# Optimization experiments

Measured on AMD Instinct MI355X. Metric: run time of the kernel, lower is better.

The kernel has to match this reference:

```python
import jax, jax.numpy as jnp
import numpy as np

B, SQ, SK = 2, 2048, 2048
D_MODEL, N_HEADS = 1024, 16
D_HEAD = D_MODEL // N_HEADS
LN_EPS = 1e-5


def _ln(x, w, b):
    # per-head LayerNorm over last dim (d_head)
    mu = jnp.mean(x, axis=-1, keepdims=True)
    var = jnp.mean(jnp.square(x - mu), axis=-1, keepdims=True)
    return (x - mu) * jax.lax.rsqrt(var + LN_EPS) * w + b


def setup_inputs() -> dict:
    key = jax.random.key(0)
    ks = jax.random.split(key, 8)
    sd = 1.0 / np.sqrt(D_MODEL)
    so = 1.0 / np.sqrt(D_HEAD)
    return {
        "x_q": jax.random.normal(ks[0], (B, SQ, D_MODEL), jnp.float32),
        "x_kv": jax.random.normal(ks[1], (B, SK, D_MODEL), jnp.float32),
        "mask": jnp.tril(jnp.ones((SQ, SK), dtype=bool)),  # causal
        "W_Q": jax.random.normal(ks[2], (N_HEADS, D_MODEL, D_HEAD), jnp.float32) * sd,
        "W_K": jax.random.normal(ks[3], (N_HEADS, D_MODEL, D_HEAD), jnp.float32) * sd,
        "W_V": jax.random.normal(ks[4], (N_HEADS, D_MODEL, D_HEAD), jnp.float32) * sd,
        "W_O": jax.random.normal(ks[5], (N_HEADS, D_HEAD, D_MODEL), jnp.float32) * so,
        "b_Q": jnp.zeros((N_HEADS, D_HEAD), jnp.float32),
        "b_K": jnp.zeros((N_HEADS, D_HEAD), jnp.float32),
        "b_V": jnp.zeros((N_HEADS, D_HEAD), jnp.float32),
        "b_O": jnp.zeros((D_MODEL,), jnp.float32),
        "ln1_w": jnp.ones((D_HEAD,), jnp.float32),
        "ln1_b": jnp.zeros((D_HEAD,), jnp.float32),
        "ln2_w": jnp.ones((D_HEAD,), jnp.float32),
        "ln2_b": jnp.zeros((D_HEAD,), jnp.float32),
    }


def reference(x_q, x_kv, mask, W_Q, W_K, W_V, W_O, b_Q, b_K, b_V, b_O,
              ln1_w, ln1_b, ln2_w, ln2_b):
    # QKV projections: b s d, n d h -> b s n h
    q = jnp.einsum('bsd,ndh->bsnh', x_q, W_Q) + b_Q
    k = jnp.einsum('bsd,ndh->bsnh', x_kv, W_K) + b_K
    v = jnp.einsum('bsd,ndh->bsnh', x_kv, W_V) + b_V
    # QK-norm (ln_first=False, rope=None -> just apply LN after projections)
    q = _ln(q, ln1_w, ln1_b)
    k = _ln(k, ln2_w, ln2_b)
    # NOTE: no 1/sqrt(d_head) scaling, matching the original module
    att = jnp.einsum('bqnh,bknh->bnqk', q, k)
    att = jnp.where(mask, att, -jnp.inf)
    probas = jax.nn.softmax(att, axis=-1)
    z = jnp.einsum('bnqk,bknh->bqnh', probas, v)
    out = jnp.einsum('bqnh,nhd->bqd', z, W_O) + b_O
    return (out, k, v)
```

## Files before the change

kernel.cpp:

```cpp
#include <hip/hip_runtime.h>
#include <hip/hip_bf16.h>

#define B_   2
#define SQ_  2048
#define DM_  1024
#define NH_  16
#define DH_  64

typedef __attribute__((ext_vector_type(8))) short          bf16x8;
typedef __attribute__((ext_vector_type(8))) unsigned short u16x8;
typedef __attribute__((ext_vector_type(4))) float          f32x4;

__device__ __forceinline__ unsigned short f2bf(float f) {
    union { __hip_bfloat16 h; unsigned short u; } c;
    c.h = __float2bfloat16(f);
    return c.u;
}
__device__ __forceinline__ float gsum16(float v) {
    v += __shfl_xor(v, 1);
    v += __shfl_xor(v, 2);
    v += __shfl_xor(v, 4);
    v += __shfl_xor(v, 8);
    return v;
}

__global__ __launch_bounds__(256) void transpose_w(
    const float* __restrict__ src, unsigned short* __restrict__ dst, int R, int C)
{
    __shared__ float t[64][65];
    const int r0 = blockIdx.x * 64, c0 = blockIdx.y * 64;
    const size_t ms = (size_t)R * C * blockIdx.z;
    src += ms; dst += ms;
    const int lr = threadIdx.x >> 6, lc = threadIdx.x & 63;
#pragma unroll
    for (int i = 0; i < 16; ++i) {
        const int row = lr + i * 4;
        t[row][lc] = src[(size_t)(r0 + row) * C + c0 + lc];
    }
    __syncthreads();
#pragma unroll
    for (int i = 0; i < 16; ++i) {
        const int crow = lr + i * 4;
        dst[(size_t)(c0 + crow) * R + r0 + lc] = f2bf(t[lc][crow]);
    }
}

template <int TN, int A_BF16, int MODE>
__global__ __launch_bounds__(256) void mfma_gemm(
    const void* __restrict__ Asrc, const unsigned short* __restrict__ WT,
    const float* __restrict__ biasK, const float* __restrict__ biasV,
    const float* __restrict__ lnw, const float* __restrict__ lnb,
    float* __restrict__ Cf, float* __restrict__ Cf2,
    unsigned short* __restrict__ Cb, unsigned short* __restrict__ CbT)
{
    constexpr int MI = (TN == 128) ? 4 : 2;
    constexpr int BP = TN / 64;

    __shared__ __align__(16) unsigned short As[128][72];
    __shared__ __align__(16) unsigned short Bs[TN][72];

    const int tid = threadIdx.x;
    const int m0 = blockIdx.y * 128;
    const int c0 = blockIdx.x * TN;

    const int srow = tid >> 2;
    const int skc  = (tid & 3) * 16;

    float4 fa[2][4];
    u16x8  ba[2][2];
    u16x8  bb[BP][2];

    const int wid = tid >> 6, lane = tid & 63;
    const int wm = (TN == 128) ? (wid >> 1) * 64 : wid * 32;
    const int wn = (TN == 128) ? (wid & 1) * 64 : 0;
    const int l15 = lane & 15, qd = lane >> 4;

    const f32x4 zero4 = {0.f, 0.f, 0.f, 0.f};
    f32x4 acc[MI][4];
#pragma unroll
    for (int mi = 0; mi < MI; ++mi)
#pragma unroll
        for (int ni = 0; ni < 4; ++ni) acc[mi][ni] = zero4;

#define LOAD_A(kb)                                                              \
    {                                                                           \
        const size_t kof = (size_t)(kb) * 64 + skc;                             \
        if constexpr (!A_BF16) {                                                \
            const float* A = (const float*)Asrc;                                \
            for (int p = 0; p < 2; ++p) {                                       \
                const float* s = A + (size_t)(m0 + srow + p * 64) * 1024 + kof; \
                fa[p][0] = *(const float4*)(s + 0);                             \
                fa[p][1] = *(const float4*)(s + 4);                             \
                fa[p][2] = *(const float4*)(s + 8);                             \
                fa[p][3] = *(const float4*)(s + 12);                            \
            }                                                                   \
        } else {                                                                \
            const unsigned short* A = (const unsigned short*)Asrc;              \
            for (int p = 0; p < 2; ++p) {                                       \
                const unsigned short* s =                                       \
                    A + (size_t)(m0 + srow + p * 64) * 1024 + kof;              \
                ba[p][0] = *(const u16x8*)(s + 0);                              \
                ba[p][1] = *(const u16x8*)(s + 8);                              \
            }                                                                   \
        }                                                                       \
        for (int p = 0; p < BP; ++p) {                                          \
            const unsigned short* s =                                           \
                WT + (size_t)(c0 + srow + p * 64) * 1024 + kof;                 \
            bb[p][0] = *(const u16x8*)(s + 0);                                  \
            bb[p][1] = *(const u16x8*)(s + 8);                                  \
        }                                                                       \
    }

    LOAD_A(0)
    for (int kb = 0; kb < 16; ++kb) {
        __syncthreads();
#pragma unroll
        for (int p = 0; p < 2; ++p) {
            if constexpr (!A_BF16) {
                u16x8 lo, hi;
                lo[0] = f2bf(fa[p][0].x); lo[1] = f2bf(fa[p][0].y);
                lo[2] = f2bf(fa[p][0].z); lo[3] = f2bf(fa[p][0].w);
                lo[4] = f2bf(fa[p][1].x); lo[5] = f2bf(fa[p][1].y);
                lo[6] = f2bf(fa[p][1].z); lo[7] = f2bf(fa[p][1].w);
                hi[0] = f2bf(fa[p][2].x); hi[1] = f2bf(fa[p][2].y);
                hi[2] = f2bf(fa[p][2].z); hi[3] = f2bf(fa[p][2].w);
                hi[4] = f2bf(fa[p][3].x); hi[5] = f2bf(fa[p][3].y);
                hi[6] = f2bf(fa[p][3].z); hi[7] = f2bf(fa[p][3].w);
                *(u16x8*)&As[srow + p * 64][skc + 0] = lo;
                *(u16x8*)&As[srow + p * 64][skc + 8] = hi;
            } else {
                *(u16x8*)&As[srow + p * 64][skc + 0] = ba[p][0];
                *(u16x8*)&As[srow + p * 64][skc + 8] = ba[p][1];
            }
        }
#pragma unroll
        for (int p = 0; p < BP; ++p) {
            *(u16x8*)&Bs[srow + p * 64][skc + 0] = bb[p][0];
            *(u16x8*)&Bs[srow + p * 64][skc + 8] = bb[p][1];
        }
        __syncthreads();
        if (kb < 15) LOAD_A(kb + 1)
#pragma unroll
        for (int ks = 0; ks < 2; ++ks) {
            bf16x8 af[MI], bfr[4];
#pragma unroll
            for (int mi = 0; mi < MI; ++mi)
                af[mi] = *(const bf16x8*)&As[wm + mi * 16 + l15][ks * 32 + qd * 8];
#pragma unroll
            for (int ni = 0; ni < 4; ++ni)
                bfr[ni] = *(const bf16x8*)&Bs[wn + ni * 16 + l15][ks * 32 + qd * 8];
#pragma unroll
            for (int mi = 0; mi < MI; ++mi)
#pragma unroll
                for (int ni = 0; ni < 4; ++ni)
                    acc[mi][ni] = __builtin_amdgcn_mfma_f32_16x16x32_bf16(
                        af[mi], bfr[ni], acc[mi][ni], 0, 0, 0);
        }
    }
#undef LOAD_A

    const float* bias = (MODE == 1 && c0 >= 1024) ? biasV : biasK;
    float bv[4];
#pragma unroll
    for (int ni = 0; ni < 4; ++ni) bv[ni] = bias[(c0 + wn + ni * 16 + l15) & 1023];
#pragma unroll
    for (int mi = 0; mi < MI; ++mi)
#pragma unroll
        for (int ni = 0; ni < 4; ++ni)
#pragma unroll
            for (int r = 0; r < 4; ++r) acc[mi][ni][r] += bv[ni];

    if constexpr (MODE != 2) {
        const bool doLN = (MODE == 0) || (c0 < 1024);
        if (doLN) {
            float w4[4], lb4[4];
#pragma unroll
            for (int ni = 0; ni < 4; ++ni) {
                w4[ni]  = lnw[ni * 16 + l15];
                lb4[ni] = lnb[ni * 16 + l15];
            }
#pragma unroll
            for (int mi = 0; mi < MI; ++mi)
#pragma unroll
                for (int r = 0; r < 4; ++r) {
                    float s1 = acc[mi][0][r] + acc[mi][1][r] + acc[mi][2][r] + acc[mi][3][r];
                    const float mu = gsum16(s1) * (1.0f / 64.0f);
                    float s2 = acc[mi][0][r] * acc[mi][0][r] + acc[mi][1][r] * acc[mi][1][r]
                             + acc[mi][2][r] * acc[mi][2][r] + acc[mi][3][r] * acc[mi][3][r];
                    const float var = gsum16(s2) * (1.0f / 64.0f) - mu * mu;
                    const float rstd = rsqrtf(var + 1e-5f);
#pragma unroll
                    for (int ni = 0; ni < 4; ++ni)
                        acc[mi][ni][r] = (acc[mi][ni][r] - mu) * rstd * w4[ni] + lb4[ni];
                }
        }
    }

    if constexpr (MODE == 0) {
#pragma unroll
        for (int mi = 0; mi < MI; ++mi)
#pragma unroll
            for (int r = 0; r < 4; ++r) {
                const size_t grow = m0 + wm + mi * 16 + qd * 4 + r;
#pragma unroll
                for (int ni = 0; ni < 4; ++ni)
                    Cb[grow * 1024 + c0 + wn + ni * 16 + l15] = f2bf(acc[mi][ni][r]);
            }
    } else if constexpr (MODE == 2) {
#pragma unroll
        for (int mi = 0; mi < MI; ++mi)
#pragma unroll
            for (int r = 0; r < 4; ++r) {
                const size_t grow = m0 + wm + mi * 16 + qd * 4 + r;
#pragma unroll
                for (int ni = 0; ni < 4; ++ni)
                    Cf[grow * 1024 + c0 + wn + ni * 16 + l15] = acc[mi][ni][r];
            }
    } else {
        if (c0 < 1024) {
#pragma unroll
            for (int mi = 0; mi < MI; ++mi)
#pragma unroll
                for (int r = 0; r < 4; ++r) {
                    const size_t grow = m0 + wm + mi * 16 + qd * 4 + r;
#pragma unroll
                    for (int ni = 0; ni < 4; ++ni) {
                        const int gcol = c0 + wn + ni * 16 + l15;
                        Cf[grow * 1024 + gcol] = acc[mi][ni][r];
                        Cb[grow * 1024 + gcol] = f2bf(acc[mi][ni][r]);
                    }
                }
        } else {
#pragma unroll
            for (int mi = 0; mi < MI; ++mi) {
                const int growb = m0 + wm + mi * 16 + qd * 4;
                const int bb_ = growb >> 11, ss = growb & 2047;
#pragma unroll
                for (int ni = 0; ni < 4; ++ni) {
                    const int gv = c0 - 1024 + wn + ni * 16 + l15;
                    const int hh = gv >> 6, dd = gv & 63;
#pragma unroll
                    for (int r = 0; r < 4; ++r)
                        Cf2[(size_t)(growb + r) * 1024 + gv] = acc[mi][ni][r];
                    ushort4 w;
                    w.x = f2bf(acc[mi][ni][0]); w.y = f2bf(acc[mi][ni][1]);
                    w.z = f2bf(acc[mi][ni][2]); w.w = f2bf(acc[mi][ni][3]);
                    *(ushort4*)&CbT[(((size_t)bb_ * NH_ + hh) * DH_ + dd) * SQ_ + ss] = w;
                }
            }
        }
    }
}

__global__ __launch_bounds__(256) void attn_mfma(
    unsigned short* __restrict__ qz, const unsigned short* __restrict__ kbf,
    const unsigned short* __restrict__ vbfT)
{
    __shared__ __align__(16) unsigned short Ks[64][72];
    __shared__ __align__(16) unsigned short VsT[64][72];
    __shared__ __align__(16) unsigned short Ps[64][72];

    const int tid = threadIdx.x;
    const int h = blockIdx.y, b = blockIdx.z;
    const int wid = tid >> 6, lane = tid & 63;
    const int l15 = lane & 15, qd = lane >> 4;
    const int srow = tid >> 2, scol = (tid & 3) * 16;

    const size_t kbase = (size_t)b * SQ_ * DM_ + (size_t)h * DH_;
    const size_t vbase = ((size_t)b * NH_ + h) * DH_ * (size_t)SQ_;

    const f32x4 zero4 = {0.f, 0.f, 0.f, 0.f};

    for (int pass = 0; pass < 2; ++pass) {
        const int qt = pass ? blockIdx.x : (SQ_ / 64 - 1) - blockIdx.x;

        bf16x8 qf[2];
        {
            const unsigned short* qp =
                qz + kbase + (size_t)(qt * 64 + wid * 16 + l15) * DM_ + qd * 8;
            qf[0] = *(const bf16x8*)(qp);
            qf[1] = *(const bf16x8*)(qp + 32);
        }

        f32x4 z[4];
#pragma unroll
        for (int ni = 0; ni < 4; ++ni) z[ni] = zero4;
        float m_i = -3.0e38f, l_i = 0.f;

        for (int kt = 0; kt <= qt; ++kt) {
            __syncthreads();
            {
                const unsigned short* ks = kbf + kbase + (size_t)(kt * 64 + srow) * DM_ + scol;
                *(u16x8*)&Ks[srow][scol + 0] = *(const u16x8*)(ks + 0);
                *(u16x8*)&Ks[srow][scol + 8] = *(const u16x8*)(ks + 8);
                const unsigned short* vs = vbfT + vbase + (size_t)srow * SQ_ + kt * 64 + scol;
                *(u16x8*)&VsT[srow][scol + 0] = *(const u16x8*)(vs + 0);
                *(u16x8*)&VsT[srow][scol + 8] = *(const u16x8*)(vs + 8);
            }
            __syncthreads();

            f32x4 s[4];
#pragma unroll
            for (int mi = 0; mi < 4; ++mi) s[mi] = zero4;
#pragma unroll
            for (int ks = 0; ks < 2; ++ks) {
#pragma unroll
                for (int mi = 0; mi < 4; ++mi) {
                    const bf16x8 af = *(const bf16x8*)&Ks[mi * 16 + l15][ks * 32 + qd * 8];
                    s[mi] = __builtin_amdgcn_mfma_f32_16x16x32_bf16(af, qf[ks], s[mi], 0, 0, 0);
                }
            }

            if (kt == qt) {
#pragma unroll
                for (int mi = 0; mi < 4; ++mi)
#pragma unroll
                    for (int r = 0; r < 4; ++r)
                        if (mi * 16 + qd * 4 + r > wid * 16 + l15) s[mi][r] = -3.0e38f;
            }

            float mloc = -3.0e38f;
#pragma unroll
            for (int mi = 0; mi < 4; ++mi)
#pragma unroll
                for (int r = 0; r < 4; ++r) mloc = fmaxf(mloc, s[mi][r]);
            mloc = fmaxf(mloc, __shfl_xor(mloc, 16));
            mloc = fmaxf(mloc, __shfl_xor(mloc, 32));
            const float mn = fmaxf(m_i, mloc);
            const float alpha = __expf(m_i - mn);
            float rs = 0.f;
#pragma unroll
            for (int mi = 0; mi < 4; ++mi)
#pragma unroll
                for (int r = 0; r < 4; ++r) {
                    const float e = __expf(s[mi][r] - mn);
                    s[mi][r] = e;
                    rs += e;
                }
            rs += __shfl_xor(rs, 16);
            rs += __shfl_xor(rs, 32);
            l_i = l_i * alpha + rs;
            m_i = mn;

#pragma unroll
            for (int mi = 0; mi < 4; ++mi) {
                ushort4 w;
                w.x = f2bf(s[mi][0]); w.y = f2bf(s[mi][1]);
                w.z = f2bf(s[mi][2]); w.w = f2bf(s[mi][3]);
                *(ushort4*)&Ps[wid * 16 + l15][mi * 16 + qd * 4] = w;
            }

#pragma unroll
            for (int r = 0; r < 4; ++r) {
                const float ar = __shfl(alpha, qd * 4 + r);
#pragma unroll
                for (int ni = 0; ni < 4; ++ni) z[ni][r] *= ar;
            }

#pragma unroll
            for (int ks = 0; ks < 2; ++ks) {
                const bf16x8 ap = *(const bf16x8*)&Ps[wid * 16 + l15][ks * 32 + qd * 8];
#pragma unroll
                for (int ni = 0; ni < 4; ++ni) {
                    const bf16x8 bv = *(const bf16x8*)&VsT[ni * 16 + l15][ks * 32 + qd * 8];
                    z[ni] = __builtin_amdgcn_mfma_f32_16x16x32_bf16(ap, bv, z[ni], 0, 0, 0);
                }
            }
        }

        const float linv = 1.0f / l_i;
#pragma unroll
        for (int r = 0; r < 4; ++r) {
            const float lr_ = __shfl(linv, qd * 4 + r);
            const size_t row = (size_t)qt * 64 + wid * 16 + qd * 4 + r;
#pragma unroll
            for (int ni = 0; ni < 4; ++ni)
                qz[kbase + row * DM_ + ni * 16 + l15] = f2bf(z[ni][r] * lr_);
        }
    }
}

extern "C" void kernel_launch(void* const* d_in, const int* in_sizes, int n_in,
                              void* d_out, int out_size, void* d_ws, size_t ws_size,
                              hipStream_t stream)
{
    const float* x_q  = (const float*)d_in[0];
    const float* x_kv = (const float*)d_in[1];
    const float* W_Q  = (const float*)d_in[3];
    const float* W_K  = (const float*)d_in[4];
    const float* W_V  = (const float*)d_in[5];
    const float* W_O  = (const float*)d_in[6];
    const float* b_Q  = (const float*)d_in[7];
    const float* b_K  = (const float*)d_in[8];
    const float* b_V  = (const float*)d_in[9];
    const float* b_O  = (const float*)d_in[10];
    const float* ln1w = (const float*)d_in[11];
    const float* ln1b = (const float*)d_in[12];
    const float* ln2w = (const float*)d_in[13];
    const float* ln2b = (const float*)d_in[14];

    const size_t NTOK = (size_t)B_ * SQ_;
    float* out  = (float*)d_out;
    float* kout = out + NTOK * DM_;
    float* vout = kout + NTOK * DM_;

    unsigned short* wsu  = (unsigned short*)d_ws;
    unsigned short* WTq  = wsu;
    unsigned short* WTkv = WTq + (1u << 20);
    unsigned short* WTo  = WTkv + (2u << 20);
    unsigned short* qz   = WTo + (1u << 20);
    unsigned short* kbf  = qz + (1u << 22);
    unsigned short* vbfT = kbf + (1u << 22);

    transpose_w<<<dim3(16, 1, 16), 256, 0, stream>>>(W_Q, WTq, 1024, 64);
    transpose_w<<<dim3(16, 1, 16), 256, 0, stream>>>(W_K, WTkv, 1024, 64);
    transpose_w<<<dim3(16, 1, 16), 256, 0, stream>>>(W_V, WTkv + (1u << 20), 1024, 64);
    transpose_w<<<dim3(16, 16, 1), 256, 0, stream>>>(W_O, WTo, 1024, 1024);

    mfma_gemm<64, 0, 0><<<dim3(16, 32), 256, 0, stream>>>(
        x_q, WTq, b_Q, nullptr, ln1w, ln1b, nullptr, nullptr, qz, nullptr);
    mfma_gemm<128, 0, 1><<<dim3(16, 32), 256, 0, stream>>>(
        x_kv, WTkv, b_K, b_V, ln2w, ln2b, kout, vout, kbf, vbfT);

    attn_mfma<<<dim3(16, NH_, B_), 256, 0, stream>>>(qz, kbf, vbfT);

    mfma_gemm<64, 1, 2><<<dim3(16, 32), 256, 0, stream>>>(
        qz, WTo, b_O, nullptr, nullptr, nullptr, out, nullptr, nullptr, nullptr);
}
```

Baseline: 278.3 us.

## Merge transposes and QKV GEMMs into single launches, widen attention query tile

The four weight-transpose launches become one kernel, and the Q and KV projection GEMMs become one fused launch of 768 blocks, with the Q path now using 128-wide tiles. The attention kernel now handles 128 query rows per block as two 64-row groups that share each K/V tile. It also prefetches the next K/V tile into registers while computing on the current one. This cuts launch count, halves K/V reloads, and overlaps global loads with compute, at the cost of more registers, a larger Ps buffer, and half as many attention blocks (256).

```diff
diff --git a/kernel.cpp b/kernel.cpp
--- a/kernel.cpp
+++ b/kernel.cpp
@@ -24,44 +24,52 @@
     return v;
 }
 
-__global__ __launch_bounds__(256) void transpose_w(
-    const float* __restrict__ src, unsigned short* __restrict__ dst, int R, int C)
+__global__ __launch_bounds__(256) void transpose_all(
+    const float* __restrict__ W_Q, const float* __restrict__ W_K,
+    const float* __restrict__ W_V, const float* __restrict__ W_O,
+    unsigned short* __restrict__ WTq, unsigned short* __restrict__ WTkv,
+    unsigned short* __restrict__ WTo)
 {
     __shared__ float t[64][65];
-    const int r0 = blockIdx.x * 64, c0 = blockIdx.y * 64;
-    const size_t ms = (size_t)R * C * blockIdx.z;
-    src += ms; dst += ms;
+    const int bid = blockIdx.x;
+    const float* src; unsigned short* dst; int R, C, r0, c0;
+    if (bid < 768) {
+        const int which = bid >> 8, rem = bid & 255;
+        const int rblk = rem & 15, zz = rem >> 4;
+        src = (which == 0) ? W_Q : (which == 1) ? W_K : W_V;
+        dst = (which == 0) ? WTq : (which == 1) ? WTkv : (WTkv + (1u << 20));
+        src += (size_t)65536 * zz;
+        dst += (size_t)65536 * zz;
+        R = 1024; C = 64; r0 = rblk * 64; c0 = 0;
+    } else {
+        const int rem = bid - 768;
+        src = W_O; dst = WTo; R = 1024; C = 1024;
+        r0 = (rem & 15) * 64; c0 = (rem >> 4) * 64;
+    }
     const int lr = threadIdx.x >> 6, lc = threadIdx.x & 63;
 #pragma unroll
-    for (int i = 0; i < 16; ++i) {
-        const int row = lr + i * 4;
-        t[row][lc] = src[(size_t)(r0 + row) * C + c0 + lc];
-    }
+    for (int i = 0; i < 16; ++i)
+        t[lr + i * 4][lc] = src[(size_t)(r0 + lr + i * 4) * C + c0 + lc];
     __syncthreads();
 #pragma unroll
-    for (int i = 0; i < 16; ++i) {
-        const int crow = lr + i * 4;
-        dst[(size_t)(c0 + crow) * R + r0 + lc] = f2bf(t[lc][crow]);
-    }
+    for (int i = 0; i < 16; ++i)
+        dst[(size_t)(c0 + lr + i * 4) * R + r0 + lc] = f2bf(t[lc][lr + i * 4]);
 }
 
 template <int TN, int A_BF16, int MODE>
-__global__ __launch_bounds__(256) void mfma_gemm(
-    const void* __restrict__ Asrc, const unsigned short* __restrict__ WT,
+__device__ __forceinline__ void gemm_body(
+    unsigned short (*__restrict__ As)[72], unsigned short (*__restrict__ Bs)[72],
+    int bx, int by, const void* __restrict__ Asrc, const unsigned short* __restrict__ WT,
     const float* __restrict__ biasK, const float* __restrict__ biasV,
     const float* __restrict__ lnw, const float* __restrict__ lnb,
     float* __restrict__ Cf, float* __restrict__ Cf2,
-    unsigned short* __restrict__ Cb, unsigned short* __restrict__ CbT)
+    unsigned short* __restrict__ Cb, unsigned short* __restrict__ CbT, int tid)
 {
     constexpr int MI = (TN == 128) ? 4 : 2;
     constexpr int BP = TN / 64;
 
-    __shared__ __align__(16) unsigned short As[128][72];
-    __shared__ __align__(16) unsigned short Bs[TN][72];
-
-    const int tid = threadIdx.x;
-    const int m0 = blockIdx.y * 128;
-    const int c0 = blockIdx.x * TN;
+    const int m0 = by * 128;
+    const int c0 = bx * TN;
 
     const int srow = tid >> 2;
     const int skc  = (tid & 3) * 16;
@@ -252,13 +260,47 @@
     }
 }
 
+__global__ __launch_bounds__(256) void qkv_fused(
+    const float* __restrict__ x_q, const float* __restrict__ x_kv,
+    const unsigned short* __restrict__ WTq, const unsigned short* __restrict__ WTkv,
+    const float* __restrict__ b_Q, const float* __restrict__ b_K,
+    const float* __restrict__ b_V,
+    const float* __restrict__ ln1w, const float* __restrict__ ln1b,
+    const float* __restrict__ ln2w, const float* __restrict__ ln2b,
+    float* __restrict__ kout, float* __restrict__ vout,
+    unsigned short* __restrict__ qz, unsigned short* __restrict__ kbf,
+    unsigned short* __restrict__ vbfT)
+{
+    __shared__ __align__(16) unsigned short As[128][72];
+    __shared__ __align__(16) unsigned short Bs[128][72];
+    const int bid = blockIdx.x, tid = threadIdx.x;
+    if (bid < 512) {
+        gemm_body<128, 0, 1>(As, Bs, bid & 15, bid >> 4, x_kv, WTkv, b_K, b_V,
+                             ln2w, ln2b, kout, vout, kbf, vbfT, tid);
+    } else {
+        const int b2 = bid - 512;
+        gemm_body<128, 0, 0>(As, Bs, b2 & 7, b2 >> 3, x_q, WTq, b_Q, nullptr,
+                             ln1w, ln1b, nullptr, nullptr, qz, nullptr, tid);
+    }
+}
+
+__global__ __launch_bounds__(256) void o_gemm(
+    const unsigned short* __restrict__ zbf, const unsigned short* __restrict__ WTo,
+    const float* __restrict__ b_O, float* __restrict__ out)
+{
+    __shared__ __align__(16) unsigned short As[128][72];
+    __shared__ __align__(16) unsigned short Bs[64][72];
+    gemm_body<64, 1, 2>(As, Bs, blockIdx.x, blockIdx.y, zbf, WTo, b_O, nullptr,
+                        nullptr, nullptr, out, nullptr, nullptr, nullptr, threadIdx.x);
+}
+
 __global__ __launch_bounds__(256) void attn_mfma(
     unsigned short* __restrict__ qz, const unsigned short* __restrict__ kbf,
     const unsigned short* __restrict__ vbfT)
 {
     __shared__ __align__(16) unsigned short Ks[64][72];
     __shared__ __align__(16) unsigned short VsT[64][72];
-    __shared__ __align__(16) unsigned short Ps[64][72];
+    __shared__ __align__(16) unsigned short Ps[128][72];
 
     const int tid = threadIdx.x;
     const int h = blockIdx.y, b = blockIdx.z;
@@ -268,114 +310,149 @@
 
     const size_t kbase = (size_t)b * SQ_ * DM_ + (size_t)h * DH_;
     const size_t vbase = ((size_t)b * NH_ + h) * DH_ * (size_t)SQ_;
-
     const f32x4 zero4 = {0.f, 0.f, 0.f, 0.f};
 
     for (int pass = 0; pass < 2; ++pass) {
-        const int qt = pass ? blockIdx.x : (SQ_ / 64 - 1) - blockIdx.x;
-
-        bf16x8 qf[2];
+        const int qt = pass ? blockIdx.x : 15 - blockIdx.x;
+
+        bf16x8 qf[2][2];
+#pragma unroll
+        for (int g = 0; g < 2; ++g) {
+            const unsigned short* qp = qz + kbase +
+                (size_t)(qt * 128 + g * 64 + wid * 16 + l15) * DM_ + qd * 8;
+            qf[g][0] = *(const bf16x8*)(qp);
+            qf[g][1] = *(const bf16x8*)(qp + 32);
+        }
+
+        f32x4 z[2][4];
+        float m_i[2], l_i[2];
+#pragma unroll
+        for (int g = 0; g < 2; ++g) {
+            m_i[g] = -3.0e38f; l_i[g] = 0.f;
+#pragma unroll
+            for (int ni = 0; ni < 4; ++ni) z[g][ni] = zero4;
+        }
+
+        const int ktmax = 2 * qt + 1;
+        u16x8 kr0, kr1, vr0, vr1;
         {
-            const unsigned short* qp =
-                qz + kbase + (size_t)(qt * 64 + wid * 16 + l15) * DM_ + qd * 8;
-            qf[0] = *(const bf16x8*)(qp);
-            qf[1] = *(const bf16x8*)(qp + 32);
-        }
-
-        f32x4 z[4];
-#pragma unroll
-        for (int ni = 0; ni < 4; ++ni) z[ni] = zero4;
-        float m_i = -3.0e38f, l_i = 0.f;
-
-        for (int kt = 0; kt <= qt; ++kt) {
+            const unsigned short* ks = kbf + kbase + (size_t)srow * DM_ + scol;
+            kr0 = *(const u16x8*)(ks);
+            kr1 = *(const u16x8*)(ks + 8);
+            const unsigned short* vs = vbfT + vbase + (size_t)srow * SQ_ + scol;
+            vr0 = *(const u16x8*)(vs);
+            vr1 = *(const u16x8*)(vs + 8);
+        }
+
+        for (int kt = 0; kt <= ktmax; ++kt) {
             __syncthreads();
-            {
-                const unsigned short* ks = kbf + kbase + (size_t)(kt * 64 + srow) * DM_ + scol;
-                *(u16x8*)&Ks[srow][scol + 0] = *(const u16x8*)(ks + 0);
-                *(u16x8*)&Ks[srow][scol + 8] = *(const u16x8*)(ks + 8);
-                const unsigned short* vs = vbfT + vbase + (size_t)srow * SQ_ + kt * 64 + scol;
-                *(u16x8*)&VsT[srow][scol + 0] = *(const u16x8*)(vs + 0);
-                *(u16x8*)&VsT[srow][scol + 8] = *(const u16x8*)(vs + 8);
-            }
+            *(u16x8*)&Ks[srow][scol + 0]  = kr0;
+            *(u16x8*)&Ks[srow][scol + 8]  = kr1;
+            *(u16x8*)&VsT[srow][scol + 0] = vr0;
+            *(u16x8*)&VsT[srow][scol + 8] = vr1;
             __syncthreads();
-
-            f32x4 s[4];
-#pragma unroll
-            for (int mi = 0; mi < 4; ++mi) s[mi] = zero4;
-#pragma unroll
-            for (int ks = 0; ks < 2; ++ks) {
+            if (kt < ktmax) {
+                const unsigned short* ks =
+                    kbf + kbase + (size_t)((kt + 1) * 64 + srow) * DM_ + scol;
+                kr0 = *(const u16x8*)(ks);
+                kr1 = *(const u16x8*)(ks + 8);
+                const unsigned short* vs =
+                    vbfT + vbase + (size_t)srow * SQ_ + (kt + 1) * 64 + scol;
+                vr0 = *(const u16x8*)(vs);
+                vr1 = *(const u16x8*)(vs + 8);
+            }
+
+#pragma unroll
+            for (int g = 0; g < 2; ++g) {
+                const int diag = 2 * qt + g;
+                if (kt > diag) continue;
+
+                f32x4 s[4];
+#pragma unroll
+                for (int mi = 0; mi < 4; ++mi) s[mi] = zero4;
+#pragma unroll
+                for (int ks2 = 0; ks2 < 2; ++ks2)
+#pragma unroll
+                    for (int mi = 0; mi < 4; ++mi) {
+                        const bf16x8 af =
+                            *(const bf16x8*)&Ks[mi * 16 + l15][ks2 * 32 + qd * 8];
+                        s[mi] = __builtin_amdgcn_mfma_f32_16x16x32_bf16(
+                            af, qf[g][ks2], s[mi], 0, 0, 0);
+                    }
+
+                if (kt == diag) {
+#pragma unroll
+                    for (int mi = 0; mi < 4; ++mi)
+#pragma unroll
+                        for (int r = 0; r < 4; ++r)
+                            if (mi * 16 + qd * 4 + r > wid * 16 + l15)
+                                s[mi][r] = -3.0e38f;
+                }
+
+                float mloc = -3.0e38f;
+#pragma unroll
+                for (int mi = 0; mi < 4; ++mi)
+#pragma unroll
+                    for (int r = 0; r < 4; ++r) mloc = fmaxf(mloc, s[mi][r]);
+                mloc = fmaxf(mloc, __shfl_xor(mloc, 16));
+                mloc = fmaxf(mloc, __shfl_xor(mloc, 32));
+                const float mn = fmaxf(m_i[g], mloc);
+                const float alpha = __expf(m_i[g] - mn);
+                float rs = 0.f;
+#pragma unroll
+                for (int mi = 0; mi < 4; ++mi)
+#pragma unroll
+                    for (int r = 0; r < 4; ++r) {
+                        const float e = __expf(s[mi][r] - mn);
+                        s[mi][r] = e;
+                        rs += e;
+                    }
+                rs += __shfl_xor(rs, 16);
+                rs += __shfl_xor(rs, 32);
+                l_i[g] = l_i[g] * alpha + rs;
+                m_i[g] = mn;
+
 #pragma unroll
                 for (int mi = 0; mi < 4; ++mi) {
-                    const bf16x8 af = *(const bf16x8*)&Ks[mi * 16 + l15][ks * 32 + qd * 8];
-                    s[mi] = __builtin_amdgcn_mfma_f32_16x16x32_bf16(af, qf[ks], s[mi], 0, 0, 0);
-                }
-            }
-
-            if (kt == qt) {
-#pragma unroll
-                for (int mi = 0; mi < 4; ++mi)
-#pragma unroll
-                    for (int r = 0; r < 4; ++r)
-                        if (mi * 16 + qd * 4 + r > wid * 16 + l15) s[mi][r] = -3.0e38f;
-            }
-
-            float mloc = -3.0e38f;
-#pragma unroll
-            for (int mi = 0; mi < 4; ++mi)
-#pragma unroll
-                for (int r = 0; r < 4; ++r) mloc = fmaxf(mloc, s[mi][r]);
-            mloc = fmaxf(mloc, __shfl_xor(mloc, 16));
-            mloc = fmaxf(mloc, __shfl_xor(mloc, 32));
-            const float mn = fmaxf(m_i, mloc);
-            const float alpha = __expf(m_i - mn);
-            float rs = 0.f;
-#pragma unroll
-            for (int mi = 0; mi < 4; ++mi)
+                    ushort4 w;
+                    w.x = f2bf(s[mi][0]); w.y = f2bf(s[mi][1]);
+                    w.z = f2bf(s[mi][2]); w.w = f2bf(s[mi][3]);
+                    *(ushort4*)&Ps[g * 64 + wid * 16 + l15][mi * 16 + qd * 4] = w;
+                }
+
 #pragma unroll
                 for (int r = 0; r < 4; ++r) {
-                    const float e = __expf(s[mi][r] - mn);
-                    s[mi][r] = e;
-                    rs += e;
-                }
-            rs += __shfl_xor(rs, 16);
-            rs += __shfl_xor(rs, 32);
-            l_i = l_i * alpha + rs;
-            m_i = mn;
-
-#pragma unroll
-            for (int mi = 0; mi < 4; ++mi) {
-                ushort4 w;
-                w.x = f2bf(s[mi][0]); w.y = f2bf(s[mi][1]);
-                w.z = f2bf(s[mi][2]); w.w = f2bf(s[mi][3]);
-                *(ushort4*)&Ps[wid * 16 + l15][mi * 16 + qd * 4] = w;
-            }
-
+                    const float ar = __shfl(alpha, qd * 4 + r);
+#pragma unroll
+                    for (int ni = 0; ni < 4; ++ni) z[g][ni][r] *= ar;
+                }
+
+#pragma unroll
+                for (int ks2 = 0; ks2 < 2; ++ks2) {
+                    const bf16x8 ap =
+                        *(const bf16x8*)&Ps[g * 64 + wid * 16 + l15][ks2 * 32 + qd * 8];
+#pragma unroll
+                    for (int ni = 0; ni < 4; ++ni) {
+                        const bf16x8 bv =
+                            *(const bf16x8*)&VsT[ni * 16 + l15][ks2 * 32 + qd * 8];
+                        z[g][ni] = __builtin_amdgcn_mfma_f32_16x16x32_bf16(
+                            ap, bv, z[g][ni], 0, 0, 0);
+                    }
+                }
+            }
+        }
+
+#pragma unroll
+        for (int g = 0; g < 2; ++g) {
+            const float linv = 1.0f / l_i[g];
 #pragma unroll
             for (int r = 0; r < 4; ++r) {
-                const float ar = __shfl(alpha, qd * 4 + r);
-#pragma unroll
-                for (int ni = 0; ni < 4; ++ni) z[ni][r] *= ar;
-            }
-
-#pragma unroll
-            for (int ks = 0; ks < 2; ++ks) {
-                const bf16x8 ap = *(const bf16x8*)&Ps[wid * 16 + l15][ks * 32 + qd * 8];
-#pragma unroll
-                for (int ni = 0; ni < 4; ++ni) {
-                    const bf16x8 bv = *(const bf16x8*)&VsT[ni * 16 + l15][ks * 32 + qd * 8];
-                    z[ni] = __builtin_amdgcn_mfma_f32_16x16x32_bf16(ap, bv, z[ni], 0, 0, 0);
-                }
-            }
-        }
-
-        const float linv = 1.0f / l_i;
-#pragma unroll
-        for (int r = 0; r < 4; ++r) {
-            const float lr_ = __shfl(linv, qd * 4 + r);
-            const size_t row = (size_t)qt * 64 + wid * 16 + qd * 4 + r;
-#pragma unroll
-            for (int ni = 0; ni < 4; ++ni)
-                qz[kbase + row * DM_ + ni * 16 + l15] = f2bf(z[ni][r] * lr_);
+                const float lr_ = __shfl(linv, qd * 4 + r);
+                const size_t row = (size_t)qt * 128 + g * 64 + wid * 16 + qd * 4 + r;
+#pragma unroll
+                for (int ni = 0; ni < 4; ++ni)
+                    qz[kbase + row * DM_ + ni * 16 + l15] = f2bf(z[g][ni][r] * lr_);
+            }
         }
     }
 }
@@ -412,18 +489,13 @@
     unsigned short* kbf  = qz + (1u << 22);
     unsigned short* vbfT = kbf + (1u << 22);
 
-    transpose_w<<<dim3(16, 1, 16), 256, 0, stream>>>(W_Q, WTq, 1024, 64);
-    transpose_w<<<dim3(16, 1, 16), 256, 0, stream>>>(W_K, WTkv, 1024, 64);
-    transpose_w<<<dim3(16, 1, 16), 256, 0, stream>>>(W_V, WTkv + (1u << 20), 1024, 64);
-    transpose_w<<<dim3(16, 16, 1), 256, 0, stream>>>(W_O, WTo, 1024, 1024);
-
-    mfma_gemm<64, 0, 0><<<dim3(16, 32), 256, 0, stream>>>(
-        x_q, WTq, b_Q, nullptr, ln1w, ln1b, nullptr, nullptr, qz, nullptr);
-    mfma_gemm<128, 0, 1><<<dim3(16, 32), 256, 0, stream>>>(
-        x_kv, WTkv, b_K, b_V, ln2w, ln2b, kout, vout, kbf, vbfT);
-
-    attn_mfma<<<dim3(16, NH_, B_), 256, 0, stream>>>(qz, kbf, vbfT);
-
-    mfma_gemm<64, 1, 2><<<dim3(16, 32), 256, 0, stream>>>(
-        qz, WTo, b_O, nullptr, nullptr, nullptr, out, nullptr, nullptr, nullptr);
-}
+    transpose_all<<<1024, 256, 0, stream>>>(W_Q, W_K, W_V, W_O, WTq, WTkv, WTo);
+
+    qkv_fused<<<768, 256, 0, stream>>>(x_q, x_kv, WTq, WTkv, b_Q, b_K, b_V,
+                                       ln1w, ln1b, ln2w, ln2b,
+                                       kout, vout, qz, kbf, vbfT);
+
+    attn_mfma<<<dim3(8, NH_, B_), 256, 0, stream>>>(qz, kbf, vbfT);
+
+    o_gemm<<<dim3(16, 32), 256, 0, stream>>>(qz, WTo, b_O, out);
+}
```

After: 290.3 us. 4.3% more time.
